# Performance work log

Measured on AMD Instinct MI355X. Metric: run time of the kernel, lower is better.

Reference implementation:

```python
import jax, jax.numpy as jnp
import numpy as np

D_MODEL = 1024
HEADS = 16
D_KEY = D_MODEL // HEADS


def setup_inputs() -> dict:
    key = jax.random.key(0)
    ks = jax.random.split(key, 7)
    B, S = 4, 2048
    queries = jax.random.normal(ks[0], (B, S, D_MODEL), dtype=jnp.float32)
    keys = jax.random.normal(ks[1], (B, S, D_MODEL), dtype=jnp.float32)
    values = jax.random.normal(ks[2], (B, S, D_MODEL), dtype=jnp.float32)
    scale = 1.0 / np.sqrt(D_MODEL)
    # Per-head projection weights, torch Linear layout [out=d_key, in=d_model], stacked over heads
    Wq = jax.random.uniform(ks[3], (HEADS, D_KEY, D_MODEL), jnp.float32, -scale, scale)
    Wk = jax.random.uniform(ks[4], (HEADS, D_KEY, D_MODEL), jnp.float32, -scale, scale)
    Wv = jax.random.uniform(ks[5], (HEADS, D_KEY, D_MODEL), jnp.float32, -scale, scale)
    Wo = jax.random.uniform(ks[6], (D_MODEL, D_MODEL), jnp.float32, -scale, scale)
    return {"queries": queries, "keys": keys, "values": values,
            "Wq": Wq, "Wk": Wk, "Wv": Wv, "Wo": Wo}


def reference(queries, keys, values, Wq, Wk, Wv, Wo):
    # Project per head: [B,S,D] x [H,K,D] -> [B,H,S,K]
    q = jnp.einsum('bsd,hkd->bhsk', queries, Wq)
    k = jnp.einsum('bsd,hkd->bhsk', keys, Wk)
    v = jnp.einsum('bsd,hkd->bhsk', values, Wv)
    attn = jnp.einsum('bhqk,bhsk->bhqs', q, k) / jnp.sqrt(jnp.float32(D_KEY))
    attn = jax.nn.softmax(attn, axis=-1)
    out = jnp.einsum('bhqs,bhsk->bhqk', attn, v)  # [B,H,S,K]
    B, H, S, K = out.shape
    # concat heads along last dim (head order = torch cat order)
    out = out.transpose(0, 2, 1, 3).reshape(B, S, H * K)
    return out @ Wo.T
```

## Files before the change

### kernel.cpp

```cpp
#include <hip/hip_runtime.h>
#include <hip/hip_bf16.h>

typedef __attribute__((ext_vector_type(8))) short short8;
typedef __attribute__((ext_vector_type(4))) short short4v;
typedef __attribute__((ext_vector_type(4))) float f32x4;
typedef __attribute__((ext_vector_type(16))) float f32x16;
typedef __bf16 bf16x8 __attribute__((ext_vector_type(8)));
typedef __attribute__((ext_vector_type(2))) unsigned int u32x2;
typedef __attribute__((ext_vector_type(4))) unsigned int u32x4;

#define DEVI static __device__ __forceinline__

DEVI short f2bs(float f) {
    union { __hip_bfloat16 h; short s; } u;
    u.h = __float2bfloat16(f);
    return u.s;
}

DEVI unsigned pack2(float a, float b) {
    union { short s[2]; unsigned u; } u;
    u.s[0] = f2bs(a);
    u.s[1] = f2bs(b);
    return u.u;
}

DEVI u32x2 pl32(unsigned x, unsigned y) {
    return __builtin_amdgcn_permlane32_swap(x, y, false, false);
}

DEVI f32x4 mfma16(short8 a, short8 b, f32x4 c) {
    return __builtin_amdgcn_mfma_f32_16x16x32_bf16(
        __builtin_bit_cast(bf16x8, a), __builtin_bit_cast(bf16x8, b), c, 0, 0, 0);
}

DEVI f32x16 mfma32(short8 a, short8 b, f32x16 c) {
    return __builtin_amdgcn_mfma_f32_32x32x16_bf16(
        __builtin_bit_cast(bf16x8, a), __builtin_bit_cast(bf16x8, b), c, 0, 0, 0);
}

DEVI void glds16(const short* g, short* l) {
    __builtin_amdgcn_global_load_lds((const __attribute__((address_space(1))) void*)g,
                                     (__attribute__((address_space(3))) void*)l, 16, 0, 0);
}

__global__ __launch_bounds__(256) void cvt_all(const float4* __restrict__ q,
                                               const float4* __restrict__ k,
                                               const float4* __restrict__ v,
                                               const float4* __restrict__ wq,
                                               const float4* __restrict__ wk,
                                               const float4* __restrict__ wv,
                                               const float4* __restrict__ wo,
                                               short4v* __restrict__ dq,
                                               short4v* __restrict__ dk,
                                               short4v* __restrict__ dv,
                                               short4v* __restrict__ dwq,
                                               short4v* __restrict__ dwk,
                                               short4v* __restrict__ dwv,
                                               short4v* __restrict__ dwo) {
    int bid = blockIdx.x;
    float4 x;
    short4v s;
    if (bid < 8192) {
        int i = bid * 256 + threadIdx.x;
        x = q[i]; s.x = f2bs(x.x); s.y = f2bs(x.y); s.z = f2bs(x.z); s.w = f2bs(x.w); dq[i] = s;
        x = k[i]; s.x = f2bs(x.x); s.y = f2bs(x.y); s.z = f2bs(x.z); s.w = f2bs(x.w); dk[i] = s;
        x = v[i]; s.x = f2bs(x.x); s.y = f2bs(x.y); s.z = f2bs(x.z); s.w = f2bs(x.w); dv[i] = s;
    } else {
        int i = (bid - 8192) * 256 + threadIdx.x;
        x = wq[i]; s.x = f2bs(x.x); s.y = f2bs(x.y); s.z = f2bs(x.z); s.w = f2bs(x.w); dwq[i] = s;
        x = wk[i]; s.x = f2bs(x.x); s.y = f2bs(x.y); s.z = f2bs(x.z); s.w = f2bs(x.w); dwk[i] = s;
        x = wv[i]; s.x = f2bs(x.x); s.y = f2bs(x.y); s.z = f2bs(x.z); s.w = f2bs(x.w); dwv[i] = s;
        x = wo[i]; s.x = f2bs(x.x); s.y = f2bs(x.y); s.z = f2bs(x.z); s.w = f2bs(x.w); dwo[i] = s;
    }
}

template <typename EpiT>
DEVI void gemm_body(const short* A, const short* Bw, short* smem, int m0, int n0, EpiT epi) {
    const int t = threadIdx.x;
    const int lane = t & 63, w = t >> 6;
    const int col = lane & 15, quad = lane >> 4;
    const int wm = (w & 1) * 64, wn = (w >> 1) * 64;

    const short* pA0;
    const short* pA1;
    const short* pB0;
    const short* pB1;
    {
        int i0 = w * 64 + lane, i1 = (4 + w) * 64 + lane;
        int L0 = i0 >> 3, cc0 = (i0 & 7) ^ (L0 & 7);
        int r0 = 2 * L0 + (cc0 & 1), c0 = cc0 >> 1;
        int L1 = i1 >> 3, cc1 = (i1 & 7) ^ (L1 & 7);
        int r1 = 2 * L1 + (cc1 & 1), c1 = cc1 >> 1;
        pA0 = A + (size_t)(m0 + r0) * 1024 + c0 * 8;
        pA1 = A + (size_t)(m0 + r1) * 1024 + c1 * 8;
        pB0 = Bw + (size_t)(n0 + r0) * 1024 + c0 * 8;
        pB1 = Bw + (size_t)(n0 + r1) * 1024 + c1 * 8;
    }
    const int posa = (2 * quad + (col & 1)) ^ (col >> 1);
    const int base_a = wm * 32 + (col >> 1) * 64 + posa * 8;
    const int base_b = wn * 32 + (col >> 1) * 64 + posa * 8;

    f32x4 acc[4][4];
#pragma unroll
    for (int i = 0; i < 4; ++i)
#pragma unroll
        for (int j = 0; j < 4; ++j) acc[i][j] = (f32x4){0.f, 0.f, 0.f, 0.f};

    glds16(pA0, smem + w * 512);
    glds16(pA1, smem + (4 + w) * 512);
    glds16(pB0, smem + 4096 + w * 512);
    glds16(pB1, smem + 4096 + (4 + w) * 512);
    pA0 += 32; pA1 += 32; pB0 += 32; pB1 += 32;
    __syncthreads();

#pragma unroll 2
    for (int kt = 0; kt < 32; ++kt) {
        const int cur = kt & 1;
        const short* Cb = smem + cur * 8192;
        if (kt < 31) {
            short* Nb = smem + (cur ^ 1) * 8192;
            glds16(pA0, Nb + w * 512);
            glds16(pA1, Nb + (4 + w) * 512);
            glds16(pB0, Nb + 4096 + w * 512);
            glds16(pB1, Nb + 4096 + (4 + w) * 512);
            pA0 += 32; pA1 += 32; pB0 += 32; pB1 += 32;
        }
        short8 a[4], b[4];
#pragma unroll
        for (int i = 0; i < 4; ++i) a[i] = *(const short8*)(Cb + base_a + i * 512);
#pragma unroll
        for (int i = 0; i < 4; ++i) b[i] = *(const short8*)(Cb + 4096 + base_b + i * 512);
        __builtin_amdgcn_s_setprio(1);
#pragma unroll
        for (int mi = 0; mi < 4; ++mi)
#pragma unroll
            for (int ni = 0; ni < 4; ++ni)
                acc[mi][ni] = mfma16(a[mi], b[ni], acc[mi][ni]);
        __builtin_amdgcn_s_setprio(0);
        __syncthreads();
    }
    epi(acc, wm, wn, col, quad);
}

__global__ __launch_bounds__(256) void qkv_gemm(const short* __restrict__ xq,
                                                const short* __restrict__ xk,
                                                const short* __restrict__ xv,
                                                const short* __restrict__ wq,
                                                const short* __restrict__ wk,
                                                const short* __restrict__ wv,
                                                short* __restrict__ qp,
                                                short* __restrict__ kp,
                                                short* __restrict__ vpt, float qscale) {
    __shared__ __align__(16) short smem[17408];
    const int lin = blockIdx.x + (blockIdx.y << 3) + (blockIdx.z << 9);
    const int wgid = (lin & 7) * 192 + (lin >> 3);
    const int n0 = (wgid & 7) * 128;
    const int m0 = ((wgid >> 3) & 63) * 128;
    const int z = wgid >> 9;
    const short* A = (z == 0) ? xq : (z == 1) ? xk : xv;
    const short* W = (z == 0) ? wq : (z == 1) ? wk : wv;

    if (z < 2) {
        short* outs = (z == 0) ? qp : kp;
        const float scale = (z == 0) ? qscale : 1.0f;
        gemm_body(A, W, smem, m0, n0, [&](f32x4 (&acc)[4][4], int wm, int wn, int col, int quad) {
            short* T = smem;
#pragma unroll
            for (int mi = 0; mi < 4; ++mi)
#pragma unroll
                for (int ni = 0; ni < 4; ++ni)
#pragma unroll
                    for (int r = 0; r < 4; ++r)
                        T[(wm + mi * 16 + quad * 4 + r) * 136 + wn + ni * 16 + col] =
                            f2bs(acc[mi][ni][r] * scale);
            __syncthreads();
            int t = threadIdx.x;
            int ml = t >> 1, nh = (t & 1) * 64;
            int m = m0 + ml;
            int b = m >> 11, s = m & 2047;
#pragma unroll
            for (int j = 0; j < 8; ++j) {
                int n = n0 + nh + j * 8;
                short8 vv = *(const short8*)(T + ml * 136 + nh + j * 8);
                size_t off = ((size_t)(b * 16 + (n >> 6)) * 2048 + s) * 64 + (n & 63);
                *(short8*)(outs + off) = vv;
            }
        });
    } else {
        gemm_body(A, W, smem, m0, n0, [&](f32x4 (&acc)[4][4], int wm, int wn, int col, int quad) {
            short* T = smem;
#pragma unroll
            for (int mi = 0; mi < 4; ++mi)
#pragma unroll
                for (int ni = 0; ni < 4; ++ni) {
                    int n_l = wn + ni * 16 + col;
                    int m_l = wm + mi * 16 + quad * 4;
                    short4v sv;
                    sv.x = f2bs(acc[mi][ni][0]); sv.y = f2bs(acc[mi][ni][1]);
                    sv.z = f2bs(acc[mi][ni][2]); sv.w = f2bs(acc[mi][ni][3]);
                    *(short4v*)(T + n_l * 132 + m_l) = sv;
                }
            __syncthreads();
            int t = threadIdx.x;
            int nrow = t >> 1, mh = (t & 1) * 64;
            int b = m0 >> 11, s0 = m0 & 2047;
            size_t base = ((size_t)(b * 1024 + n0 + nrow)) * 2048 + s0 + mh;
#pragma unroll
            for (int j = 0; j < 16; ++j) {
                unsigned long long vv = *(const unsigned long long*)(T + nrow * 132 + mh + j * 4);
                *(unsigned long long*)(vpt + base + j * 4) = vv;
            }
        });
    }
}

__global__ __launch_bounds__(256) void out_gemm(const short* __restrict__ ao,
                                                const short* __restrict__ wo,
                                                float* __restrict__ outf) {
    __shared__ __align__(16) short smem[16896];
    const int lin = blockIdx.x + (blockIdx.y << 3);
    const int wgid = (lin & 7) * 64 + (lin >> 3);
    const int n0 = (wgid & 7) * 128;
    const int m0 = (wgid >> 3) * 128;
    gemm_body(ao, wo, smem, m0, n0, [&](f32x4 (&acc)[4][4], int wm, int wn, int col, int quad) {
#pragma unroll
        for (int mi = 0; mi < 4; ++mi)
#pragma unroll
            for (int ni = 0; ni < 4; ++ni)
#pragma unroll
                for (int r = 0; r < 4; ++r) {
                    int m = m0 + wm + mi * 16 + quad * 4 + r;
                    int n = n0 + wn + ni * 16 + col;
                    outf[(size_t)m * 1024 + n] = acc[mi][ni][r];
                }
    });
}

__global__ __launch_bounds__(256, 4) void flash_attn(const short* __restrict__ qp,
                                                     const short* __restrict__ kp,
                                                     const short* __restrict__ vpt,
                                                     short* __restrict__ ao) {
    __shared__ __align__(16) short smem[16384];
    short* Ks2 = smem;
    short* Vs2 = smem + 8192;

    const int t = threadIdx.x, lane = t & 63, w = t >> 6;
    const int rl = lane & 31, hi = lane >> 5;
    const int bh = blockIdx.x, q0 = blockIdx.y * 128;
    const short* qb = qp + (size_t)bh * 2048 * 64;
    const short* kb = kp + (size_t)bh * 2048 * 64;
    const short* vb = vpt + (size_t)bh * 64 * 2048;

#pragma unroll
    for (int j = 0; j < 4; ++j) {
        int cbase = (j * 4 + w) * 64;
        int c = cbase + lane;
        int row = c >> 3, kc = (c & 7) ^ ((row >> 1) & 7);
        glds16(qb + (size_t)(q0 + row) * 64 + kc * 8, smem + cbase * 8);
    }
    __syncthreads();

    int offA[4];
#pragma unroll
    for (int j = 0; j < 4; ++j) offA[j] = (((j * 2 + hi) ^ ((rl >> 1) & 7)) * 8) + rl * 64;

    short8 bQ0 = *(const short8*)(smem + w * 2048 + offA[0]);
    short8 bQ1 = *(const short8*)(smem + w * 2048 + offA[1]);
    short8 bQ2 = *(const short8*)(smem + w * 2048 + offA[2]);
    short8 bQ3 = *(const short8*)(smem + w * 2048 + offA[3]);
    __syncthreads();

    const short* kg0;
    const short* kg1;
    const short* vg0;
    const short* vg1;
    {
        int c0 = w * 64 + lane, c1 = (4 + w) * 64 + lane;
        int r0 = c0 >> 3, p0 = c0 & 7, r1 = c1 >> 3, p1 = c1 & 7;
        int kc0 = p0 ^ ((r0 >> 1) & 7), kc1 = p1 ^ ((r1 >> 1) & 7);
        kg0 = kb + r0 * 64 + kc0 * 8;
        kg1 = kb + r1 * 64 + kc1 * 8;
        vg0 = vb + (size_t)r0 * 2048 + kc0 * 8;
        vg1 = vb + (size_t)r1 * 2048 + kc1 * 8;
    }

    const f32x16 kZ = {0.f, 0.f, 0.f, 0.f, 0.f, 0.f, 0.f, 0.f,
                       0.f, 0.f, 0.f, 0.f, 0.f, 0.f, 0.f, 0.f};
    f32x16 acc_o0 = kZ, acc_o1 = kZ, acc_l = kZ;
    const short ONE = 0x3F80;
    const short8 vones = {ONE, ONE, ONE, ONE, ONE, ONE, ONE, ONE};

    glds16(kg0, Ks2 + w * 512);
    glds16(kg1, Ks2 + (4 + w) * 512);
    glds16(vg0, Vs2 + w * 512);
    glds16(vg1, Vs2 + (4 + w) * 512);
    kg0 += 4096; kg1 += 4096; vg0 += 64; vg1 += 64;
    __syncthreads();

#pragma unroll 2
    for (int kt = 0; kt < 32; ++kt) {
        const int cur = kt & 1;
        if (kt < 31) {
            const int nxt = cur ^ 1;
            glds16(kg0, Ks2 + nxt * 4096 + w * 512);
            glds16(kg1, Ks2 + nxt * 4096 + (4 + w) * 512);
            glds16(vg0, Vs2 + nxt * 4096 + w * 512);
            glds16(vg1, Vs2 + nxt * 4096 + (4 + w) * 512);
            kg0 += 4096; kg1 += 4096; vg0 += 64; vg1 += 64;
        }
        const short* Ks = Ks2 + cur * 4096;
        const short* Vs = Vs2 + cur * 4096;

#pragma unroll
        for (int g = 0; g < 2; ++g) {
            const short* Kg = Ks + g * 2048;
            __builtin_amdgcn_s_setprio(1);
            short8 a0 = *(const short8*)(Kg + offA[0]);
            f32x16 st = mfma32(a0, bQ0, kZ);
            short8 a1k = *(const short8*)(Kg + offA[1]);
            st = mfma32(a1k, bQ1, st);
            short8 a2k = *(const short8*)(Kg + offA[2]);
            st = mfma32(a2k, bQ2, st);
            short8 a3k = *(const short8*)(Kg + offA[3]);
            st = mfma32(a3k, bQ3, st);
            __builtin_amdgcn_s_setprio(0);

            unsigned d0 = pack2(__builtin_amdgcn_exp2f(st[0]), __builtin_amdgcn_exp2f(st[1]));
            unsigned d1 = pack2(__builtin_amdgcn_exp2f(st[2]), __builtin_amdgcn_exp2f(st[3]));
            unsigned d2 = pack2(__builtin_amdgcn_exp2f(st[4]), __builtin_amdgcn_exp2f(st[5]));
            unsigned d3 = pack2(__builtin_amdgcn_exp2f(st[6]), __builtin_amdgcn_exp2f(st[7]));
            u32x2 t02 = pl32(d0, d2);
            u32x2 t13 = pl32(d1, d3);
            u32x4 a1v = {t02[0], t13[0], t02[1], t13[1]};
            short8 pA1 = __builtin_bit_cast(short8, a1v);
            __builtin_amdgcn_s_setprio(1);
            short8 bv00 = *(const short8*)(Vs + offA[g * 2]);
            acc_o0 = mfma32(pA1, bv00, acc_o0);
            short8 bv01 = *(const short8*)(Vs + 2048 + offA[g * 2]);
            acc_o1 = mfma32(pA1, bv01, acc_o1);
            acc_l = mfma32(pA1, vones, acc_l);
            __builtin_amdgcn_s_setprio(0);

            unsigned d4 = pack2(__builtin_amdgcn_exp2f(st[8]), __builtin_amdgcn_exp2f(st[9]));
            unsigned d5 = pack2(__builtin_amdgcn_exp2f(st[10]), __builtin_amdgcn_exp2f(st[11]));
            unsigned d6 = pack2(__builtin_amdgcn_exp2f(st[12]), __builtin_amdgcn_exp2f(st[13]));
            unsigned d7 = pack2(__builtin_amdgcn_exp2f(st[14]), __builtin_amdgcn_exp2f(st[15]));
            u32x2 t46 = pl32(d4, d6);
            u32x2 t57 = pl32(d5, d7);
            u32x4 a2v = {t46[0], t57[0], t46[1], t57[1]};
            short8 pA2 = __builtin_bit_cast(short8, a2v);
            __builtin_amdgcn_s_setprio(1);
            short8 bv10 = *(const short8*)(Vs + offA[g * 2 + 1]);
            acc_o0 = mfma32(pA2, bv10, acc_o0);
            short8 bv11 = *(const short8*)(Vs + 2048 + offA[g * 2 + 1]);
            acc_o1 = mfma32(pA2, bv11, acc_o1);
            acc_l = mfma32(pA2, vones, acc_l);
            __builtin_amdgcn_s_setprio(0);
        }
        __syncthreads();
    }

    const int b = bh >> 4, hd = bh & 15;
#pragma unroll
    for (int r = 0; r < 16; ++r) {
        float inv = 1.0f / acc_l[r];
        int qrow = q0 + w * 32 + (r & 3) + 8 * (r >> 2) + 4 * hi;
        size_t base = ((size_t)(b * 2048 + qrow)) * 1024 + hd * 64 + rl;
        ao[base] = f2bs(acc_o0[r] * inv);
        ao[base + 32] = f2bs(acc_o1[r] * inv);
    }
}

extern "C" void kernel_launch(void* const* d_in, const int* in_sizes, int n_in,
                              void* d_out, int out_size, void* d_ws, size_t ws_size,
                              hipStream_t stream) {
    const float* q  = (const float*)d_in[0];
    const float* k  = (const float*)d_in[1];
    const float* v  = (const float*)d_in[2];
    const float* Wq = (const float*)d_in[3];
    const float* Wk = (const float*)d_in[4];
    const float* Wv = (const float*)d_in[5];
    const float* Wo = (const float*)d_in[6];
    float* out = (float*)d_out;

    short* ws = (short*)d_ws;
    const size_t SZ = (size_t)64 * 2048 * 64;
    const size_t WZ = (size_t)1024 * 1024;
    short* xq  = ws;
    short* xk  = ws + SZ;
    short* xv  = ws + 2 * SZ;
    short* qp  = ws + 3 * SZ;
    short* kp  = ws + 4 * SZ;
    short* wqb = ws + 5 * SZ;
    short* wkb = wqb + WZ;
    short* wvb = wqb + 2 * WZ;
    short* wob = wqb + 3 * WZ;
    short* ao  = xq;
    short* vpt = (short*)d_out;

    const float QSCALE = 0.125f * 1.44269504088896f;

    cvt_all<<<dim3(9216), dim3(256), 0, stream>>>(
        (const float4*)q, (const float4*)k, (const float4*)v, (const float4*)Wq,
        (const float4*)Wk, (const float4*)Wv, (const float4*)Wo, (short4v*)xq, (short4v*)xk,
        (short4v*)xv, (short4v*)wqb, (short4v*)wkb, (short4v*)wvb, (short4v*)wob);
    dim3 blk(256);
    qkv_gemm<<<dim3(8, 64, 3), blk, 0, stream>>>(xq, xk, xv, wqb, wkb, wvb, qp, kp, vpt, QSCALE);
    flash_attn<<<dim3(64, 16), blk, 0, stream>>>(qp, kp, vpt, ao);
    out_gemm<<<dim3(8, 64), blk, 0, stream>>>(ao, wob, out);
}
```

Before: 343.2 us.

## Triple-buffer GEMM K-loop with explicit vmcnt waits and single barrier

Replaces the double-buffered K loop in the shared GEMM body with a three-stage LDS ring. Two tiles are prefetched ahead, and each iteration uses a partial vmcnt wait plus one barrier before issuing the next load and computing. The aim is to hide global-to-LDS latency better and drop the trailing per-iteration syncthreads. LDS use per block grows to 48KB, which may reduce occupancy. Correctness also depends on the vmcnt counts matching the four loads issued per stage.

```diff
diff --git a/kernel.cpp b/kernel.cpp
--- a/kernel.cpp
+++ b/kernel.cpp
@@ -106,40 +106,63 @@
 #pragma unroll
         for (int j = 0; j < 4; ++j) acc[i][j] = (f32x4){0.f, 0.f, 0.f, 0.f};
 
-    glds16(pA0, smem + w * 512);
-    glds16(pA1, smem + (4 + w) * 512);
-    glds16(pB0, smem + 4096 + w * 512);
-    glds16(pB1, smem + 4096 + (4 + w) * 512);
-    pA0 += 32; pA1 += 32; pB0 += 32; pB1 += 32;
+#define STAGE(BUF)                                          \
+    do {                                                    \
+        short* Nb = smem + (BUF)*8192;                      \
+        glds16(pA0, Nb + w * 512);                          \
+        glds16(pA1, Nb + (4 + w) * 512);                    \
+        glds16(pB0, Nb + 4096 + w * 512);                   \
+        glds16(pB1, Nb + 4096 + (4 + w) * 512);             \
+        pA0 += 32; pA1 += 32; pB0 += 32; pB1 += 32;         \
+    } while (0)
+
+#define COMPUTE(BUF)                                                                \
+    do {                                                                            \
+        const short* Cb = smem + (BUF)*8192;                                        \
+        short8 a[4], b[4];                                                          \
+        _Pragma("unroll") for (int i = 0; i < 4; ++i)                               \
+            a[i] = *(const short8*)(Cb + base_a + i * 512);                         \
+        _Pragma("unroll") for (int i = 0; i < 4; ++i)                               \
+            b[i] = *(const short8*)(Cb + 4096 + base_b + i * 512);                  \
+        __builtin_amdgcn_s_setprio(1);                                              \
+        _Pragma("unroll") for (int mi = 0; mi < 4; ++mi)                            \
+            _Pragma("unroll") for (int ni = 0; ni < 4; ++ni)                        \
+                acc[mi][ni] = mfma16(a[mi], b[ni], acc[mi][ni]);                    \
+        __builtin_amdgcn_s_setprio(0);                                              \
+    } while (0)
+
+#define ITER(CUR, NXT)                                      \
+    do {                                                    \
+        asm volatile("s_waitcnt vmcnt(4)" ::: "memory");    \
+        __builtin_amdgcn_s_barrier();                       \
+        __builtin_amdgcn_sched_barrier(0);                  \
+        STAGE(NXT);                                         \
+        COMPUTE(CUR);                                       \
+    } while (0)
+
+    STAGE(0);
+    STAGE(1);
+
+#pragma unroll 1
+    for (int b3 = 0; b3 < 10; ++b3) {
+        ITER(0, 2);
+        ITER(1, 0);
+        ITER(2, 1);
+    }
+    asm volatile("s_waitcnt vmcnt(4)" ::: "memory");
+    __builtin_amdgcn_s_barrier();
+    __builtin_amdgcn_sched_barrier(0);
+    COMPUTE(0);
+    asm volatile("s_waitcnt vmcnt(0)" ::: "memory");
+    __builtin_amdgcn_s_barrier();
+    __builtin_amdgcn_sched_barrier(0);
+    COMPUTE(1);
+
     __syncthreads();
-
-#pragma unroll 2
-    for (int kt = 0; kt < 32; ++kt) {
-        const int cur = kt & 1;
-        const short* Cb = smem + cur * 8192;
-        if (kt < 31) {
-            short* Nb = smem + (cur ^ 1) * 8192;
-            glds16(pA0, Nb + w * 512);
-            glds16(pA1, Nb + (4 + w) * 512);
-            glds16(pB0, Nb + 4096 + w * 512);
-            glds16(pB1, Nb + 4096 + (4 + w) * 512);
-            pA0 += 32; pA1 += 32; pB0 += 32; pB1 += 32;
-        }
-        short8 a[4], b[4];
-#pragma unroll
-        for (int i = 0; i < 4; ++i) a[i] = *(const short8*)(Cb + base_a + i * 512);
-#pragma unroll
-        for (int i = 0; i < 4; ++i) b[i] = *(const short8*)(Cb + 4096 + base_b + i * 512);
-        __builtin_amdgcn_s_setprio(1);
-#pragma unroll
-        for (int mi = 0; mi < 4; ++mi)
-#pragma unroll
-            for (int ni = 0; ni < 4; ++ni)
-                acc[mi][ni] = mfma16(a[mi], b[ni], acc[mi][ni]);
-        __builtin_amdgcn_s_setprio(0);
-        __syncthreads();
-    }
     epi(acc, wm, wn, col, quad);
+#undef ITER
+#undef COMPUTE
+#undef STAGE
 }
 
 __global__ __launch_bounds__(256) void qkv_gemm(const short* __restrict__ xq,
@@ -151,7 +174,7 @@
                                                 short* __restrict__ qp,
                                                 short* __restrict__ kp,
                                                 short* __restrict__ vpt, float qscale) {
-    __shared__ __align__(16) short smem[17408];
+    __shared__ __align__(16) short smem[24576];
     const int lin = blockIdx.x + (blockIdx.y << 3) + (blockIdx.z << 9);
     const int wgid = (lin & 7) * 192 + (lin >> 3);
     const int n0 = (wgid & 7) * 128;
@@ -217,7 +240,7 @@
 __global__ __launch_bounds__(256) void out_gemm(const short* __restrict__ ao,
                                                 const short* __restrict__ wo,
                                                 float* __restrict__ outf) {
-    __shared__ __align__(16) short smem[16896];
+    __shared__ __align__(16) short smem[24576];
     const int lin = blockIdx.x + (blockIdx.y << 3);
     const int wgid = (lin & 7) * 64 + (lin >> 3);
     const int n0 = (wgid & 7) * 128;
```

New measurement: 343.2 us. About the same (+0.0%).
